# Optimization experiments

Hardware: AMD Instinct MI355X
Metric: run time of the kernel (lower is better)

## Reference

```python
import jax, jax.numpy as jnp
import numpy as np
from jax import lax

B, S, Q, A, L = 8192, 8192, 64, 1024, 3
H = 64  # post-processor hidden


def setup_inputs() -> dict:
    key = jax.random.key(0)
    ks = jax.random.split(key, 9)
    state = jax.random.normal(ks[0], (B, S), dtype=jnp.float32)
    enc_w = jax.random.normal(ks[1], (Q, S), dtype=jnp.float32) * (1.0 / np.sqrt(S))
    enc_b = jnp.zeros((Q,), dtype=jnp.float32)
    quantum_params = jax.random.normal(ks[2], (L, Q, 3), dtype=jnp.float32) * 0.1
    measurement_ops = jax.random.normal(ks[3], (A, Q, 2), dtype=jnp.float32) * 0.1
    w1 = jax.random.normal(ks[4], (H, A), dtype=jnp.float32) * (1.0 / np.sqrt(A))
    b1 = jnp.zeros((H,), dtype=jnp.float32)
    w2 = jax.random.normal(ks[5], (A, H), dtype=jnp.float32) * (1.0 / np.sqrt(H))
    b2 = jnp.zeros((A,), dtype=jnp.float32)
    return {"state": state, "enc_w": enc_w, "enc_b": enc_b,
            "quantum_params": quantum_params, "measurement_ops": measurement_ops,
            "w1": w1, "b1": b1, "w2": w2, "b2": b2}


def reference(state, enc_w, enc_b, quantum_params, measurement_ops, w1, b1, w2, b2):
    # Encode: Linear + softmax. quantum_state = complex(encoded, 0); since every
    # rotation is a real scaling (qs*cos + roll(qs)*sin), the imaginary part
    # stays identically zero, so we track only the real component.
    encoded = jax.nn.softmax(state @ enc_w.T + enc_b, axis=-1)  # [B, Q]

    # Rotation gates applied sequentially in layer -> qubit -> (x,y,z) order,
    # which is exactly the row-major flattening of quantum_params.
    thetas = quantum_params.reshape(-1)  # [L*Q*3]

    def gate(qs, theta):
        c = jnp.cos(theta * 0.5)
        s = jnp.sin(theta * 0.5)
        return qs * c + jnp.roll(qs, 1, axis=-1) * s, None

    qs, _ = lax.scan(gate, encoded, thetas)  # [B, Q]

    # Measurement: torch.sum has no dim -> reduces over batch AND qubit dims.
    # imag == 0, so the ops[:, :, 1] term contributes nothing.
    measurements = jnp.einsum('bq,aq->a', qs, measurement_ops[:, :, 0])  # [A]

    # Post-processor MLP on the [A] vector.
    h = jax.nn.relu(measurements @ w1.T + b1)
    return h @ w2.T + b2  # [A]
```

## Files before the change

### kernel.cpp

```cpp
#include <hip/hip_runtime.h>
#include <hip/hip_fp16.h>

typedef __fp16 h2_t __attribute__((ext_vector_type(2)));
typedef _Float16 f16x8 __attribute__((ext_vector_type(8)));
typedef float f32x4 __attribute__((ext_vector_type(4)));
typedef unsigned int uint32;

#define S_DIM 8192
#define B_DIM 8192
#define Q_DIM 64
#define A_DIM 1024
#define H_DIM 64
#define N_GATES 576

#define MT 64
#define KSPLIT 8
#define KC (S_DIM / KSPLIT)
#define BK 32
#define NSTEP (KC / BK)
#define NCHUNK 4
#define CHUNK (N_GATES / NCHUNK)

__device__ __forceinline__ uint32 pk_f16(float x, float y) {
    h2_t h = __builtin_amdgcn_cvt_pkrtz(x, y);
    return __builtin_bit_cast(uint32, h);
}

__device__ __forceinline__ f32x4 mfma16(uint4 a, uint4 b, f32x4 c) {
    return __builtin_amdgcn_mfma_f32_16x16x32_f16(
        __builtin_bit_cast(f16x8, a), __builtin_bit_cast(f16x8, b), c, 0, 0, 0);
}

__device__ __forceinline__ void gload_lds16(const float* g, float* lds) {
    __builtin_amdgcn_global_load_lds(
        (const __attribute__((address_space(1))) void*)g,
        (__attribute__((address_space(3))) void*)lds, 16, 0, 0);
}

__global__ void k_pre(const float* __restrict__ encw, uint4* __restrict__ bpack,
                      const float* __restrict__ w1, const float* __restrict__ mo,
                      float* __restrict__ WM) {
    const int bid = blockIdx.x;
    const int t   = threadIdx.x;
    if (bid < 256) {
        const int gid  = bid * 256 + t;
        const int lane = gid & 63;
        const int nt   = (gid >> 6) & 3;
        const int kt   = gid >> 8;
        const int n = nt * 16 + (lane & 15);
        const int k = kt * 32 + (lane >> 4) * 8;
        const float* p = encw + (size_t)n * S_DIM + k;
        float4 x0 = *(const float4*)p;
        float4 x1 = *(const float4*)(p + 4);
        uint4 r;
        r.x = pk_f16(x0.x, x0.y);
        r.y = pk_f16(x0.z, x0.w);
        r.z = pk_f16(x1.x, x1.y);
        r.w = pk_f16(x1.z, x1.w);
        bpack[gid] = r;
    } else {
        __shared__ float red[4][64];
        const int j    = bid - 256;
        const int lane = t & 63;
        const int wv   = t >> 6;
        const float* w1r = w1 + (size_t)j * A_DIM + wv * 256;
        const float* mop = mo + (size_t)wv * 256 * 128 + lane * 2;
        float acc = 0.f;
#pragma unroll 8
        for (int a = 0; a < 256; ++a)
            acc = fmaf(w1r[a], mop[(size_t)a * 128], acc);
        red[wv][lane] = acc;
        __syncthreads();
        if (t < 64)
            WM[(size_t)j * 64 + t] = red[0][t] + red[1][t] + red[2][t] + red[3][t];
    }
}

__global__ __launch_bounds__(256, 4) void k_gemm(
        const float* __restrict__ state, const uint4* __restrict__ bpack,
        float* __restrict__ partial) {
    __shared__ __align__(16) float As[3][MT * BK];
    __shared__ __align__(16) float Bs[3][4 * 256];
    const int t  = threadIdx.x;
    const int w  = t >> 6;
    const int l  = t & 63;
    const int m0 = blockIdx.x * MT;
    const int ks = blockIdx.y;
    const int k0 = ks * KC;

    const int fr = w * 16 + (l & 15);
    const int fx = fr & 7;
    const int g2 = l >> 4;

#define DMA(BUF, S) do { \
        _Pragma("unroll") \
        for (int i = 0; i < 2; ++i) { \
            const int j_ = 2 * w + i; \
            const int rl = j_ * 8 + (l >> 3); \
            const int ss = (l & 7) ^ (l >> 3); \
            const float* gp = state + (size_t)(m0 + rl) * S_DIM + k0 + (S) * BK + ss * 4; \
            gload_lds16(gp, &As[BUF][j_ * 256]); \
        } \
        { \
            const float* gb = (const float*)(bpack + (size_t)((k0 >> 5) + (S)) * 256 + w * 64 + l); \
            gload_lds16(gb, &Bs[BUF][w * 256]); \
        } } while (0)

#define COMPUTE(BUF, S) do { \
        const int b0 = fr * BK; \
        const float4 f0 = *(const float4*)&As[BUF][b0 + (((2 * g2 + 0) ^ fx) << 2)]; \
        const float4 f1 = *(const float4*)&As[BUF][b0 + (((2 * g2 + 1) ^ fx) << 2)]; \
        uint4 af; \
        af.x = pk_f16(f0.x, f0.y); af.y = pk_f16(f0.z, f0.w); \
        af.z = pk_f16(f1.x, f1.y); af.w = pk_f16(f1.z, f1.w); \
        const uint4 bf0 = *(const uint4*)&Bs[BUF][0 * 256 + l * 4]; \
        const uint4 bf1 = *(const uint4*)&Bs[BUF][1 * 256 + l * 4]; \
        const uint4 bf2 = *(const uint4*)&Bs[BUF][2 * 256 + l * 4]; \
        const uint4 bf3 = *(const uint4*)&Bs[BUF][3 * 256 + l * 4]; \
        acc[0] = mfma16(af, bf0, acc[0]); \
        acc[1] = mfma16(af, bf1, acc[1]); \
        acc[2] = mfma16(af, bf2, acc[2]); \
        acc[3] = mfma16(af, bf3, acc[3]); } while (0)

    f32x4 acc[4] = {};

    DMA(0, 0);
    DMA(1, 1);

    int buf = 0, ibuf = 2;
    for (int s = 0; s < NSTEP - 1; ++s) {
        asm volatile("s_waitcnt vmcnt(3)" ::: "memory");
        __builtin_amdgcn_s_barrier();
        __builtin_amdgcn_sched_barrier(0);
        if (s + 2 < NSTEP) DMA(ibuf, s + 2);
        COMPUTE(buf, s);
        buf  = (buf  == 2) ? 0 : buf  + 1;
        ibuf = (ibuf == 2) ? 0 : ibuf + 1;
    }
    asm volatile("s_waitcnt vmcnt(0)" ::: "memory");
    __builtin_amdgcn_s_barrier();
    __builtin_amdgcn_sched_barrier(0);
    COMPUTE(buf, NSTEP - 1);
#undef DMA
#undef COMPUTE

    float* pc = partial + (size_t)ks * (B_DIM * Q_DIM);
    const int mr = m0 + w * 16 + (l >> 4) * 4;
    const int nc = l & 15;
#pragma unroll
    for (int nt = 0; nt < 4; ++nt)
#pragma unroll
        for (int r = 0; r < 4; ++r)
            pc[(size_t)(mr + r) * Q_DIM + nt * 16 + nc] = acc[nt][r];
}

__global__ void k_softmax(const float* __restrict__ partial,
                          const float* __restrict__ encb,
                          float* __restrict__ colsum_parts) {
    __shared__ float red[4][64];
    const int lane = threadIdx.x & 63;
    const int wv   = threadIdx.x >> 6;
    const float eb = encb[lane];
    float accq = 0.f;
    for (int i = 0; i < 8; ++i) {
        const int r = blockIdx.x * 32 + i * 4 + wv;
        float x = eb;
#pragma unroll
        for (int ks = 0; ks < KSPLIT; ++ks)
            x += partial[(size_t)ks * (B_DIM * Q_DIM) + (size_t)r * Q_DIM + lane];
        float m = x;
        for (int o = 32; o > 0; o >>= 1) m = fmaxf(m, __shfl_xor(m, o));
        float e = __expf(x - m);
        float s = e;
        for (int o = 32; o > 0; o >>= 1) s += __shfl_xor(s, o);
        accq += e / s;
    }
    red[wv][lane] = accq;
    __syncthreads();
    if (threadIdx.x < 64) {
        colsum_parts[blockIdx.x * 64 + lane] =
            red[0][lane] + red[1][lane] + red[2][lane] + red[3][lane];
    }
}

__global__ void k_final(const float* __restrict__ colsum_parts,
                        const float* __restrict__ qp,
                        const float* __restrict__ WM,
                        const float* __restrict__ b1,
                        const float* __restrict__ w2, const float* __restrict__ b2,
                        float* __restrict__ out) {
    __shared__ float red[4][64];
    __shared__ float t0[64];
    __shared__ float cs[N_GATES], ss[N_GATES];
    __shared__ float pA[NCHUNK][64];
    __shared__ float pB[2][64];
    __shared__ float fv[64];
    __shared__ float gv[64];
    __shared__ float hl[64];
    const int t    = threadIdx.x;
    const int lane = t & 63;
    const int wv   = t >> 6;

    for (int g = t; g < N_GATES; g += 256) {
        float th = qp[g] * 0.5f;
        cs[g] = __cosf(th);
        ss[g] = __sinf(th);
    }
    {
        float c = 0.f;
#pragma unroll
        for (int i = 0; i < 64; ++i)
            c += colsum_parts[(size_t)(wv * 64 + i) * 64 + lane];
        red[wv][lane] = c;
    }
    __syncthreads();
    if (t < 64)
        t0[t] = red[0][t] + red[1][t] + red[2][t] + red[3][t];
    {
        float p = (lane == 0) ? 1.f : 0.f;
        const int g0 = wv * CHUNK;
        for (int g = 0; g < CHUNK; ++g) {
            float prev = __shfl(p, (lane + 63) & 63);
            p = fmaf(cs[g0 + g], p, ss[g0 + g] * prev);
        }
        pA[wv][lane] = p;
    }
    __syncthreads();
    if (wv < 2) {
        float r = 0.f;
        for (int i = 0; i < 64; ++i)
            r += pA[2 * wv][i] * pA[2 * wv + 1][(lane - i) & 63];
        pB[wv][lane] = r;
    }
    __syncthreads();
    if (wv == 0) {
        float r = 0.f;
        for (int i = 0; i < 64; ++i)
            r += pB[0][i] * pB[1][(lane - i) & 63];
        fv[lane] = r;
    }
    __syncthreads();
    if (wv == 0) {
        float r = 0.f;
        for (int i = 0; i < 64; ++i)
            r += fv[i] * t0[(lane - i) & 63];
        gv[lane] = r;
    }
    __syncthreads();
    if (t < 64) {
        float v = 0.f;
        const float* wr = WM + (size_t)t * 64;
#pragma unroll
        for (int q = 0; q < 64; ++q)
            v = fmaf(wr[q], gv[q], v);
        hl[t] = fmaxf(v + b1[t], 0.f);
    }
    __syncthreads();
    const int a = blockIdx.x * 4 + wv;
    float v = w2[(size_t)a * H_DIM + lane] * hl[lane];
    for (int o = 32; o > 0; o >>= 1) v += __shfl_xor(v, o);
    if (lane == 0) out[a] = v + b2[a];
}

extern "C" void kernel_launch(void* const* d_in, const int* in_sizes, int n_in,
                              void* d_out, int out_size, void* d_ws, size_t ws_size,
                              hipStream_t stream) {
    const float* state = (const float*)d_in[0];
    const float* encw  = (const float*)d_in[1];
    const float* encb  = (const float*)d_in[2];
    const float* qp    = (const float*)d_in[3];
    const float* mo    = (const float*)d_in[4];
    const float* w1    = (const float*)d_in[5];
    const float* b1    = (const float*)d_in[6];
    const float* w2    = (const float*)d_in[7];
    const float* b2    = (const float*)d_in[8];
    float* out = (float*)d_out;

    float* ws           = (float*)d_ws;
    float* colsum_parts = ws;
    float* partial      = ws + 16384;
    float* WM           = partial + (size_t)KSPLIT * B_DIM * Q_DIM;
    uint4* bpack        = (uint4*)(WM + 4096);

    k_pre<<<dim3(320), dim3(256), 0, stream>>>(encw, bpack, w1, mo, WM);
    k_gemm<<<dim3(B_DIM / MT, KSPLIT), dim3(256), 0, stream>>>(state, bpack, partial);
    k_softmax<<<dim3(256), dim3(256), 0, stream>>>(partial, encb, colsum_parts);
    k_final<<<dim3(256), dim3(256), 0, stream>>>(colsum_parts, qp, WM, b1, w2, b2, out);
}
```

Before: 86.90 us.

## Keep full B k-slice resident in LDS and loop four M-tiles per block

The GEMM block now preloads its entire packed encoder-weight k-slice (128 KB) into LDS once, then processes four consecutive 64-row M-tiles, streaming only the state tiles through a triple buffer. Accumulators are written out and reset every 32 steps. This removes the repeated per-step B reloads and cuts redundant B traffic by a factor of four. In exchange the large LDS footprint allows only one block per CU and the grid shrinks to 256 blocks, so there is much less latency hiding and less parallelism.

```diff
diff --git a/kernel.cpp b/kernel.cpp
--- a/kernel.cpp
+++ b/kernel.cpp
@@ -14,10 +14,11 @@
 #define N_GATES 576
 
 #define MT 64
+#define LMT 4
 #define KSPLIT 8
 #define KC (S_DIM / KSPLIT)
 #define BK 32
-#define NSTEP (KC / BK)
+#define NST (LMT * KC / BK)
 #define NCHUNK 4
 #define CHUNK (N_GATES / NCHUNK)
 
@@ -76,82 +77,96 @@
     }
 }
 
-__global__ __launch_bounds__(256, 4) void k_gemm(
+__global__ __launch_bounds__(256, 1) void k_gemm(
         const float* __restrict__ state, const uint4* __restrict__ bpack,
         float* __restrict__ partial) {
     __shared__ __align__(16) float As[3][MT * BK];
-    __shared__ __align__(16) float Bs[3][4 * 256];
+    __shared__ __align__(16) uint4 Bs[(KC / 32) * 256];
     const int t  = threadIdx.x;
     const int w  = t >> 6;
     const int l  = t & 63;
-    const int m0 = blockIdx.x * MT;
-    const int ks = blockIdx.y;
-    const int k0 = ks * KC;
+    const int m0b = blockIdx.x * (MT * LMT);
+    const int ks  = blockIdx.y;
+    const int k0  = ks * KC;
 
     const int fr = w * 16 + (l & 15);
     const int fx = fr & 7;
     const int g2 = l >> 4;
 
+    {
+        const uint4* pbsrc = bpack + (size_t)(k0 >> 5) * 256;
+#pragma unroll 4
+        for (int c = 0; c < 32; ++c) {
+            const int ch = w * 32 + c;
+            gload_lds16((const float*)(pbsrc + ch * 64 + l), (float*)&Bs[ch * 64]);
+        }
+    }
+
 #define DMA(BUF, S) do { \
+        const int mt_ = (S) >> 5; \
+        const int kf_ = ((S) & 31) * BK; \
         _Pragma("unroll") \
         for (int i = 0; i < 2; ++i) { \
             const int j_ = 2 * w + i; \
             const int rl = j_ * 8 + (l >> 3); \
             const int ss = (l & 7) ^ (l >> 3); \
-            const float* gp = state + (size_t)(m0 + rl) * S_DIM + k0 + (S) * BK + ss * 4; \
+            const float* gp = state + (size_t)(m0b + mt_ * MT + rl) * S_DIM + k0 + kf_ + ss * 4; \
             gload_lds16(gp, &As[BUF][j_ * 256]); \
-        } \
-        { \
-            const float* gb = (const float*)(bpack + (size_t)((k0 >> 5) + (S)) * 256 + w * 64 + l); \
-            gload_lds16(gb, &Bs[BUF][w * 256]); \
         } } while (0)
-
-#define COMPUTE(BUF, S) do { \
-        const int b0 = fr * BK; \
-        const float4 f0 = *(const float4*)&As[BUF][b0 + (((2 * g2 + 0) ^ fx) << 2)]; \
-        const float4 f1 = *(const float4*)&As[BUF][b0 + (((2 * g2 + 1) ^ fx) << 2)]; \
-        uint4 af; \
-        af.x = pk_f16(f0.x, f0.y); af.y = pk_f16(f0.z, f0.w); \
-        af.z = pk_f16(f1.x, f1.y); af.w = pk_f16(f1.z, f1.w); \
-        const uint4 bf0 = *(const uint4*)&Bs[BUF][0 * 256 + l * 4]; \
-        const uint4 bf1 = *(const uint4*)&Bs[BUF][1 * 256 + l * 4]; \
-        const uint4 bf2 = *(const uint4*)&Bs[BUF][2 * 256 + l * 4]; \
-        const uint4 bf3 = *(const uint4*)&Bs[BUF][3 * 256 + l * 4]; \
-        acc[0] = mfma16(af, bf0, acc[0]); \
-        acc[1] = mfma16(af, bf1, acc[1]); \
-        acc[2] = mfma16(af, bf2, acc[2]); \
-        acc[3] = mfma16(af, bf3, acc[3]); } while (0)
 
     f32x4 acc[4] = {};
 
     DMA(0, 0);
     DMA(1, 1);
-
-    int buf = 0, ibuf = 2;
-    for (int s = 0; s < NSTEP - 1; ++s) {
-        asm volatile("s_waitcnt vmcnt(3)" ::: "memory");
+    asm volatile("s_waitcnt vmcnt(4)" ::: "memory");
+    __builtin_amdgcn_s_barrier();
+
+    int buf = 0;
+    for (int s = 0; s < NST; ++s) {
+        if (s < NST - 2) {
+            asm volatile("s_waitcnt vmcnt(2)" ::: "memory");
+        } else {
+            asm volatile("s_waitcnt vmcnt(0)" ::: "memory");
+        }
         __builtin_amdgcn_s_barrier();
         __builtin_amdgcn_sched_barrier(0);
-        if (s + 2 < NSTEP) DMA(ibuf, s + 2);
-        COMPUTE(buf, s);
-        buf  = (buf  == 2) ? 0 : buf  + 1;
-        ibuf = (ibuf == 2) ? 0 : ibuf + 1;
-    }
-    asm volatile("s_waitcnt vmcnt(0)" ::: "memory");
-    __builtin_amdgcn_s_barrier();
-    __builtin_amdgcn_sched_barrier(0);
-    COMPUTE(buf, NSTEP - 1);
+        if (s + 2 < NST) {
+            const int ib = (buf == 0) ? 2 : buf - 1;
+            DMA(ib, s + 2);
+        }
+        {
+            const int kt = s & 31;
+            const int b0 = fr * BK;
+            const float4 f0 = *(const float4*)&As[buf][b0 + (((2 * g2 + 0) ^ fx) << 2)];
+            const float4 f1 = *(const float4*)&As[buf][b0 + (((2 * g2 + 1) ^ fx) << 2)];
+            uint4 af;
+            af.x = pk_f16(f0.x, f0.y); af.y = pk_f16(f0.z, f0.w);
+            af.z = pk_f16(f1.x, f1.y); af.w = pk_f16(f1.z, f1.w);
+            const uint4 bf0 = Bs[kt * 256 + 0 * 64 + l];
+            const uint4 bf1 = Bs[kt * 256 + 1 * 64 + l];
+            const uint4 bf2 = Bs[kt * 256 + 2 * 64 + l];
+            const uint4 bf3 = Bs[kt * 256 + 3 * 64 + l];
+            acc[0] = mfma16(af, bf0, acc[0]);
+            acc[1] = mfma16(af, bf1, acc[1]);
+            acc[2] = mfma16(af, bf2, acc[2]);
+            acc[3] = mfma16(af, bf3, acc[3]);
+        }
+        if ((s & 31) == 31) {
+            const int mt = s >> 5;
+            float* pc = partial + (size_t)ks * (B_DIM * Q_DIM);
+            const int mr = m0b + mt * MT + w * 16 + (l >> 4) * 4;
+            const int nc = l & 15;
+#pragma unroll
+            for (int nt = 0; nt < 4; ++nt) {
+#pragma unroll
+                for (int r = 0; r < 4; ++r)
+                    pc[(size_t)(mr + r) * Q_DIM + nt * 16 + nc] = acc[nt][r];
+                acc[nt] = (f32x4){0.f, 0.f, 0.f, 0.f};
+            }
+        }
+        buf = (buf == 2) ? 0 : buf + 1;
+    }
 #undef DMA
-#undef COMPUTE
-
-    float* pc = partial + (size_t)ks * (B_DIM * Q_DIM);
-    const int mr = m0 + w * 16 + (l >> 4) * 4;
-    const int nc = l & 15;
-#pragma unroll
-    for (int nt = 0; nt < 4; ++nt)
-#pragma unroll
-        for (int r = 0; r < 4; ++r)
-            pc[(size_t)(mr + r) * Q_DIM + nt * 16 + nc] = acc[nt][r];
 }
 
 __global__ void k_softmax(const float* __restrict__ partial,
@@ -283,7 +298,7 @@
     uint4* bpack        = (uint4*)(WM + 4096);
 
     k_pre<<<dim3(320), dim3(256), 0, stream>>>(encw, bpack, w1, mo, WM);
-    k_gemm<<<dim3(B_DIM / MT, KSPLIT), dim3(256), 0, stream>>>(state, bpack, partial);
+    k_gemm<<<dim3(B_DIM / (MT * LMT), KSPLIT), dim3(256), 0, stream>>>(state, bpack, partial);
     k_softmax<<<dim3(256), dim3(256), 0, stream>>>(partial, encb, colsum_parts);
     k_final<<<dim3(256), dim3(256), 0, stream>>>(colsum_parts, qp, WM, b1, w2, b2, out);
 }
```

Measured after the change: 166.4 us. 1.91x slower.
